# Performance work log

Measured on AMD Instinct MI355X. Metric: run time of the kernel, lower is better.

## Reference

```python
import itertools
import jax, jax.numpy as jnp
import numpy as np

B, S, D = 512, 49, 448
H, KD, RATIO, RES = 8, 32, 4, 7
EKD = KD * RATIO              # expanded key dim = 128
QKV_OUT = H * (2 * KD + EKD)  # 1536
MLP_HID = D * 4               # 1792
EPS = 1e-5
LS_INIT = 1e-5


def _build_bias_idxs():
    points = list(itertools.product(range(RES), range(RES)))
    offsets = {}
    idxs = []
    for p1 in points:
        for p2 in points:
            off = (abs(p1[0] - p2[0]), abs(p1[1] - p2[1]))
            if off not in offsets:
                offsets[off] = len(offsets)
            idxs.append(offsets[off])
    return np.asarray(idxs, dtype=np.int32).reshape(len(points), len(points)), len(offsets)


def setup_inputs() -> dict:
    key = jax.random.key(0)
    ks = jax.random.split(key, 10)
    idxs_np, n_off = _build_bias_idxs()  # (49,49), 49 unique offsets
    std = 0.02
    return {
        "hidden_states": jax.random.normal(ks[0], (B, S, D), jnp.float32),
        "ln1_g": jnp.ones((D,), jnp.float32),
        "ln1_b": jnp.zeros((D,), jnp.float32),
        "qkv_w": jax.random.normal(ks[1], (D, QKV_OUT), jnp.float32) * std,
        "qkv_b": jnp.zeros((QKV_OUT,), jnp.float32),
        "attention_biases": jax.random.normal(ks[2], (H, n_off), jnp.float32) * std,
        "proj_w": jax.random.normal(ks[3], (H * EKD, D), jnp.float32) * std,
        "proj_b": jnp.zeros((D,), jnp.float32),
        "ln2_g": jnp.ones((D,), jnp.float32),
        "ln2_b": jnp.zeros((D,), jnp.float32),
        "mlp_w1": jax.random.normal(ks[4], (D, MLP_HID), jnp.float32) * std,
        "mlp_b1": jnp.zeros((MLP_HID,), jnp.float32),
        "mlp_w2": jax.random.normal(ks[5], (MLP_HID, D), jnp.float32) * std,
        "mlp_b2": jnp.zeros((D,), jnp.float32),
        "ls1": jnp.full((D,), LS_INIT, jnp.float32),
        "ls2": jnp.full((D,), LS_INIT, jnp.float32),
        "attention_bias_idxs": jnp.asarray(idxs_np),
    }


def _layernorm(x, g, b):
    mu = jnp.mean(x, axis=-1, keepdims=True)
    var = jnp.mean(jnp.square(x - mu), axis=-1, keepdims=True)
    return (x - mu) * jax.lax.rsqrt(var + EPS) * g + b


def reference(hidden_states, ln1_g, ln1_b, qkv_w, qkv_b, attention_biases,
              proj_w, proj_b, ln2_g, ln2_b, mlp_w1, mlp_b1, mlp_w2, mlp_b2,
              ls1, ls2, attention_bias_idxs):
    x = hidden_states
    # --- token mixer (self-attention with relative-position bias) ---
    h = _layernorm(x, ln1_g, ln1_b)
    qkv = h @ qkv_w + qkv_b                           # [B,S,1536]
    qkv = qkv.reshape(B, S, H, 2 * KD + EKD)
    q, k, v = jnp.split(qkv, [KD, 2 * KD], axis=3)    # [B,S,H,32/32/128]
    scale = KD ** (-0.5)
    scores = jnp.einsum("bqhd,bkhd->bhqk", q, k) * scale
    bias = attention_biases[:, attention_bias_idxs]   # [H,S,S]
    probs = jax.nn.softmax(scores + bias[None], axis=-1)
    ctx = jnp.einsum("bhqk,bkhd->bqhd", probs, v).reshape(B, S, H * EKD)
    attn_out = ctx @ proj_w + proj_b                  # [B,S,D]
    # --- residual with layerscale (drop_path = identity in eval) ---
    x = x + ls1 * attn_out
    # --- MLP branch ---
    h2 = _layernorm(x, ln2_g, ln2_b)
    m = jax.nn.gelu(h2 @ mlp_w1 + mlp_b1, approximate=False)
    m = m @ mlp_w2 + mlp_b2
    x = x + ls2 * m
    return x
```

## Files before the change

kernel.cpp:

```cpp
#include <hip/hip_runtime.h>
#include <hip/hip_bf16.h>

#define BB 512
#define SS 49
#define DD 448
#define HH 8
#define QKVO 1536
#define MLPH 1792
#define MM (BB*SS)

using bf16_t = __hip_bfloat16;
typedef __attribute__((ext_vector_type(8))) short short8;
typedef __attribute__((ext_vector_type(4))) float f32x4;

__device__ __forceinline__ void gload_lds16(const void* g, void* l) {
  __builtin_amdgcn_global_load_lds(
      (const __attribute__((address_space(1))) void*)g,
      (__attribute__((address_space(3))) void*)l,
      16, 0, 0);
}

__global__ void prep_kernel(const float* __restrict__ qkv_w, const float* __restrict__ proj_w,
                            const float* __restrict__ w1, const float* __restrict__ w2,
                            const float* __restrict__ ab, const int* __restrict__ idxs,
                            bf16_t* __restrict__ qkv_wT, bf16_t* __restrict__ proj_wT,
                            bf16_t* __restrict__ w1T, bf16_t* __restrict__ w2T,
                            bf16_t* __restrict__ bias_pad)
{
  int idx = blockIdx.x * 256 + threadIdx.x;
  if (idx < 688128) {
    int n = idx / 448, k = idx % 448;
    qkv_wT[idx] = __float2bfloat16(qkv_w[k*1536 + n]);
  } else if ((idx -= 688128) < 458752) {
    int n = idx / 1024, k = idx % 1024;
    proj_wT[idx] = __float2bfloat16(proj_w[k*448 + n]);
  } else if ((idx -= 458752) < 802816) {
    int n = idx / 448, k = idx % 448;
    w1T[idx] = __float2bfloat16(w1[k*1792 + n]);
  } else if ((idx -= 802816) < 802816) {
    int n = idx / 1792, k = idx % 1792;
    w2T[idx] = __float2bfloat16(w2[k*448 + n]);
  } else if ((idx -= 802816) < 32768) {
    int h = idx >> 12, r = (idx >> 6) & 63, c = idx & 63;
    float v = (r < SS && c < SS) ? ab[h*49 + idxs[r*49 + c]] : -1e30f;
    bias_pad[idx] = __float2bfloat16(v);
  }
}

__global__ __launch_bounds__(256) void ln_kernel(const float* __restrict__ x,
                                                 const float* __restrict__ g,
                                                 const float* __restrict__ b,
                                                 bf16_t* __restrict__ out)
{
  const int w = threadIdx.x >> 6, lane = threadIdx.x & 63;
  const int row = blockIdx.x * 4 + w;
  const float* xr = x + (size_t)row * DD;
  float v[7];
  float s = 0.f;
#pragma unroll
  for (int j = 0; j < 7; ++j) { v[j] = xr[lane + 64*j]; s += v[j]; }
#pragma unroll
  for (int off = 32; off; off >>= 1) s += __shfl_xor(s, off, 64);
  const float mu = s * (1.0f/448.0f);
  float q = 0.f;
#pragma unroll
  for (int j = 0; j < 7; ++j) { float d = v[j] - mu; q += d*d; }
#pragma unroll
  for (int off = 32; off; off >>= 1) q += __shfl_xor(q, off, 64);
  const float rstd = rsqrtf(q * (1.0f/448.0f) + 1e-5f);
  bf16_t* orow = out + (size_t)row * DD;
#pragma unroll
  for (int j = 0; j < 7; ++j) {
    int c = lane + 64*j;
    orow[c] = __float2bfloat16((v[j] - mu) * rstd * g[c] + b[c]);
  }
}

enum { EP_BF16 = 0, EP_RES1 = 1, EP_GELU = 2, EP_RES2 = 3 };

template<int EPI>
__global__ __launch_bounds__(256, 2) void gemm_bf16(
    const bf16_t* __restrict__ A, const bf16_t* __restrict__ Bt,
    const float* __restrict__ bias, const float* __restrict__ resid,
    const float* __restrict__ ls, bf16_t* __restrict__ Obf,
    float* __restrict__ Of, int N, int K)
{
  __shared__ __align__(16) char lds[32768];
  const int t = threadIdx.x;
  const int lane = t & 63;
  const int w = t >> 6;
  const int m0 = blockIdx.x * 128;
  const int n0 = blockIdx.y * 128;
  const int fr = lane & 15;
  const int fq = lane >> 4;
  const int wm = (w >> 1) * 64;
  const int wn = (w & 1) * 64;

  f32x4 acc[4][4];
#pragma unroll
  for (int i = 0; i < 4; ++i)
#pragma unroll
    for (int j = 0; j < 4; ++j)
      acc[i][j] = f32x4{0.f, 0.f, 0.f, 0.f};

  const int rsub = t >> 3;
  const int g8 = (t & 7) ^ (rsub & 7);
  const int wbase = (t & 192) * 16;
  const int nkt = K >> 6;

  for (int kt = 0; kt < nkt; ++kt) {
    const int k0 = kt << 6;
#pragma unroll
    for (int i = 0; i < 4; ++i) {
      const int ra = i*32 + rsub;
      gload_lds16(A + (size_t)(m0 + ra) * K + (k0 + g8*8), lds + i*4096 + wbase);
      int rb = n0 + i*32 + rsub;
      if (rb >= N) rb = N - 1;
      gload_lds16(Bt + (size_t)rb * K + (k0 + g8*8), lds + 16384 + i*4096 + wbase);
    }
    __syncthreads();
#pragma unroll
    for (int kk = 0; kk < 2; ++kk) {
      short8 af[4], bfr[4];
#pragma unroll
      for (int i = 0; i < 4; ++i) {
        const int ra = wm + i*16 + fr;
        const int ca = (fq + kk*4) ^ (ra & 7);
        af[i] = *(const short8*)(lds + ra*128 + ca*16);
        const int rb2 = wn + i*16 + fr;
        const int cb = (fq + kk*4) ^ (rb2 & 7);
        bfr[i] = *(const short8*)(lds + 16384 + rb2*128 + cb*16);
      }
#pragma unroll
      for (int mi = 0; mi < 4; ++mi)
#pragma unroll
        for (int ni = 0; ni < 4; ++ni)
          acc[mi][ni] = __builtin_amdgcn_mfma_f32_16x16x32_bf16(af[mi], bfr[ni], acc[mi][ni], 0, 0, 0);
    }
    __syncthreads();
  }

#pragma unroll
  for (int mi = 0; mi < 4; ++mi) {
#pragma unroll
    for (int ni = 0; ni < 4; ++ni) {
      const int col = n0 + wn + ni*16 + fr;
      if (col < N) {
        const float bc = bias[col];
        const int row0 = m0 + wm + mi*16 + fq*4;
#pragma unroll
        for (int ri = 0; ri < 4; ++ri) {
          const size_t o = (size_t)(row0 + ri) * N + col;
          const float v = acc[mi][ni][ri] + bc;
          if constexpr (EPI == EP_BF16) {
            Obf[o] = __float2bfloat16(v);
          } else if constexpr (EPI == EP_GELU) {
            Obf[o] = __float2bfloat16(0.5f * v * (1.0f + erff(v * 0.7071067811865475f)));
          } else if constexpr (EPI == EP_RES1) {
            Of[o] = resid[o] + ls[col] * v;
          } else {
            Of[o] = Of[o] + ls[col] * v;
          }
        }
      }
    }
  }
}

__global__ __launch_bounds__(64) void attn_mfma_kernel(const bf16_t* __restrict__ qkv,
                                                       const bf16_t* __restrict__ bias_pad,
                                                       bf16_t* __restrict__ ctx)
{
  __shared__ __align__(16) bf16_t VsF[64*128];
  __shared__ __align__(16) bf16_t PsF[64*72];
  const int b = blockIdx.x >> 3, h = blockIdx.x & 7;
  const int l = threadIdx.x;
  const int fr = l & 15, g = l >> 4;
  const size_t base = ((size_t)b * SS) * QKVO + (size_t)h * 192;

  for (int c = l; c < 1024; c += 64) {
    const int j = c >> 4, ch = c & 15;
    const int jc = j < SS ? j : SS - 1;
    short8 v = *(const short8*)(qkv + base + (size_t)jc * QKVO + 64 + ch*8);
    *(short8*)(&VsF[j*128 + ((ch ^ (j >> 3)) & 15)*8]) = v;
  }

  short8 qf[4], kf[4];
#pragma unroll
  for (int mi = 0; mi < 4; ++mi) {
    int qr = mi*16 + fr; if (qr > SS-1) qr = SS-1;
    qf[mi] = *(const short8*)(qkv + base + (size_t)qr * QKVO + g*8);
    int kr = mi*16 + fr; if (kr > SS-1) kr = SS-1;
    kf[mi] = *(const short8*)(qkv + base + (size_t)kr * QKVO + 32 + g*8);
  }
  f32x4 sc[4][4];
#pragma unroll
  for (int mi = 0; mi < 4; ++mi)
#pragma unroll
    for (int ni = 0; ni < 4; ++ni)
      sc[mi][ni] = f32x4{0.f,0.f,0.f,0.f};
#pragma unroll
  for (int mi = 0; mi < 4; ++mi)
#pragma unroll
    for (int ni = 0; ni < 4; ++ni)
      sc[mi][ni] = __builtin_amdgcn_mfma_f32_16x16x32_bf16(qf[mi], kf[ni], sc[mi][ni], 0, 0, 0);

  const float scale = 0.17677669529663687f;
  const bf16_t* bp = bias_pad + (size_t)h * 4096;
#pragma unroll
  for (int mi = 0; mi < 4; ++mi) {
#pragma unroll
    for (int ri = 0; ri < 4; ++ri) {
      const int r = mi*16 + g*4 + ri;
      float v0 = sc[mi][0][ri]*scale + __bfloat162float(bp[r*64 +      fr]);
      float v1 = sc[mi][1][ri]*scale + __bfloat162float(bp[r*64 + 16 + fr]);
      float v2 = sc[mi][2][ri]*scale + __bfloat162float(bp[r*64 + 32 + fr]);
      float v3 = sc[mi][3][ri]*scale + __bfloat162float(bp[r*64 + 48 + fr]);
      float m = fmaxf(fmaxf(v0, v1), fmaxf(v2, v3));
#pragma unroll
      for (int off = 8; off; off >>= 1) m = fmaxf(m, __shfl_xor(m, off, 64));
      v0 = __expf(v0 - m); v1 = __expf(v1 - m);
      v2 = __expf(v2 - m); v3 = __expf(v3 - m);
      float s = v0 + v1 + v2 + v3;
#pragma unroll
      for (int off = 8; off; off >>= 1) s += __shfl_xor(s, off, 64);
      const float inv = 1.0f / s;
      PsF[r*72 +      fr] = __float2bfloat16(v0 * inv);
      PsF[r*72 + 16 + fr] = __float2bfloat16(v1 * inv);
      PsF[r*72 + 32 + fr] = __float2bfloat16(v2 * inv);
      PsF[r*72 + 48 + fr] = __float2bfloat16(v3 * inv);
    }
  }
  __syncthreads();

  short8 pf[4][2];
#pragma unroll
  for (int mi = 0; mi < 4; ++mi)
#pragma unroll
    for (int ks = 0; ks < 2; ++ks)
      pf[mi][ks] = *(const short8*)(&PsF[(mi*16 + fr)*72 + ks*32 + g*8]);

#pragma unroll
  for (int ni = 0; ni < 8; ++ni) {
    const int e = ni*16 + fr;
    short8 vf[2];
#pragma unroll
    for (int ks = 0; ks < 2; ++ks) {
      const int jb = ks*32 + g*8;
#pragma unroll
      for (int jj = 0; jj < 8; ++jj) {
        const int j = jb + jj;
        const int ch = ((e >> 3) ^ (j >> 3)) & 15;
        vf[ks][jj] = *(const short*)(&VsF[j*128 + ch*8 + (e & 7)]);
      }
    }
    f32x4 acc2[4];
#pragma unroll
    for (int mi = 0; mi < 4; ++mi) acc2[mi] = f32x4{0.f,0.f,0.f,0.f};
#pragma unroll
    for (int ks = 0; ks < 2; ++ks)
#pragma unroll
      for (int mi = 0; mi < 4; ++mi)
        acc2[mi] = __builtin_amdgcn_mfma_f32_16x16x32_bf16(pf[mi][ks], vf[ks], acc2[mi], 0, 0, 0);
#pragma unroll
    for (int mi = 0; mi < 4; ++mi) {
#pragma unroll
      for (int ri = 0; ri < 4; ++ri) {
        const int q = mi*16 + g*4 + ri;
        if (q < SS)
          ctx[((size_t)b * SS + q) * 1024 + h*128 + e] = __float2bfloat16(acc2[mi][ri]);
      }
    }
  }
}

extern "C" void kernel_launch(void* const* d_in, const int* in_sizes, int n_in,
                              void* d_out, int out_size, void* d_ws, size_t ws_size,
                              hipStream_t stream) {
  const float* x      = (const float*)d_in[0];
  const float* ln1_g  = (const float*)d_in[1];
  const float* ln1_b  = (const float*)d_in[2];
  const float* qkv_w  = (const float*)d_in[3];
  const float* qkv_b  = (const float*)d_in[4];
  const float* ab     = (const float*)d_in[5];
  const float* proj_w = (const float*)d_in[6];
  const float* proj_b = (const float*)d_in[7];
  const float* ln2_g  = (const float*)d_in[8];
  const float* ln2_b  = (const float*)d_in[9];
  const float* w1     = (const float*)d_in[10];
  const float* b1     = (const float*)d_in[11];
  const float* w2     = (const float*)d_in[12];
  const float* b2     = (const float*)d_in[13];
  const float* ls1    = (const float*)d_in[14];
  const float* ls2    = (const float*)d_in[15];
  const int*   idxs   = (const int*)d_in[16];
  float* out = (float*)d_out;
  char* ws = (char*)d_ws;

  bf16_t* h_buf    = (bf16_t*)(ws);
  bf16_t* qkv_buf  = (bf16_t*)(ws + 22478848);
  bf16_t* ctx_buf  = (bf16_t*)(ws + 99549184);
  bf16_t* m_buf    = (bf16_t*)(ws + 22478848);
  bf16_t* qkv_wT   = (bf16_t*)(ws + 150929408);
  bf16_t* proj_wT  = (bf16_t*)(ws + 152305664);
  bf16_t* w1T      = (bf16_t*)(ws + 153223168);
  bf16_t* w2T      = (bf16_t*)(ws + 154828800);
  bf16_t* bias_pad = (bf16_t*)(ws + 156434432);

  const int prep_total = 688128 + 458752 + 802816 + 802816 + 32768;
  prep_kernel<<<(prep_total + 255)/256, 256, 0, stream>>>(
      qkv_w, proj_w, w1, w2, ab, idxs, qkv_wT, proj_wT, w1T, w2T, bias_pad);

  ln_kernel<<<MM/4, 256, 0, stream>>>(x, ln1_g, ln1_b, h_buf);

  gemm_bf16<EP_BF16><<<dim3(MM/128, 12), 256, 0, stream>>>(
      h_buf, qkv_wT, qkv_b, nullptr, nullptr, qkv_buf, nullptr, QKVO, DD);

  attn_mfma_kernel<<<BB*HH, 64, 0, stream>>>(qkv_buf, bias_pad, ctx_buf);

  gemm_bf16<EP_RES1><<<dim3(MM/128, 4), 256, 0, stream>>>(
      ctx_buf, proj_wT, proj_b, x, ls1, nullptr, out, DD, 1024);

  ln_kernel<<<MM/4, 256, 0, stream>>>(out, ln2_g, ln2_b, h_buf);

  gemm_bf16<EP_GELU><<<dim3(MM/128, 14), 256, 0, stream>>>(
      h_buf, w1T, b1, nullptr, nullptr, m_buf, nullptr, MLPH, DD);

  gemm_bf16<EP_RES2><<<dim3(MM/128, 4), 256, 0, stream>>>(
      m_buf, w2T, b2, nullptr, ls2, nullptr, out, DD, MLPH);
}
```

Measured before the change: 342.9 us.

## Use 256x256 pipelined 8-wave GEMM and tiled transpose for weight prep

Replaces the 128x128 4-wave GEMM with a 256x256 tile, 512-thread kernel. It uses a 4-stage LDS ring buffer (128KB of dynamic shared memory), prefetches two K-steps ahead with direct global-to-LDS loads, and interleaves the half-tile loads with MFMA bursts under explicit barriers and priority hints. Weight transposes move from an uncoalesced gather kernel to an LDS-tiled transpose-cast. The larger tiles leave fewer blocks and waste columns on N=448 (the 2x256 grid pads to 512), and the 128KB of LDS may restrict occupancy to one block per CU.

Result: slower. 407.8 us (+19.0%).

```diff
diff --git a/kernel.cpp b/kernel.cpp
--- a/kernel.cpp
+++ b/kernel.cpp
@@ -20,31 +20,30 @@
       16, 0, 0);
 }
 
-__global__ void prep_kernel(const float* __restrict__ qkv_w, const float* __restrict__ proj_w,
-                            const float* __restrict__ w1, const float* __restrict__ w2,
-                            const float* __restrict__ ab, const int* __restrict__ idxs,
-                            bf16_t* __restrict__ qkv_wT, bf16_t* __restrict__ proj_wT,
-                            bf16_t* __restrict__ w1T, bf16_t* __restrict__ w2T,
-                            bf16_t* __restrict__ bias_pad)
+__global__ __launch_bounds__(256) void transpose_cast(const float* __restrict__ src,
+                                                      bf16_t* __restrict__ dst,
+                                                      int R, int C)
+{
+  __shared__ float tile[32][33];
+  const int tx = threadIdx.x & 31, ty = threadIdx.x >> 5;
+  const int c0 = blockIdx.x * 32, r0 = blockIdx.y * 32;
+#pragma unroll
+  for (int i = 0; i < 4; ++i)
+    tile[ty + i*8][tx] = src[(size_t)(r0 + ty + i*8) * C + c0 + tx];
+  __syncthreads();
+#pragma unroll
+  for (int i = 0; i < 4; ++i)
+    dst[(size_t)(c0 + ty + i*8) * R + r0 + tx] = __float2bfloat16(tile[tx][ty + i*8]);
+}
+
+__global__ __launch_bounds__(256) void biasprep_kernel(const float* __restrict__ ab,
+                                                       const int* __restrict__ idxs,
+                                                       bf16_t* __restrict__ bias_pad)
 {
   int idx = blockIdx.x * 256 + threadIdx.x;
-  if (idx < 688128) {
-    int n = idx / 448, k = idx % 448;
-    qkv_wT[idx] = __float2bfloat16(qkv_w[k*1536 + n]);
-  } else if ((idx -= 688128) < 458752) {
-    int n = idx / 1024, k = idx % 1024;
-    proj_wT[idx] = __float2bfloat16(proj_w[k*448 + n]);
-  } else if ((idx -= 458752) < 802816) {
-    int n = idx / 448, k = idx % 448;
-    w1T[idx] = __float2bfloat16(w1[k*1792 + n]);
-  } else if ((idx -= 802816) < 802816) {
-    int n = idx / 1792, k = idx % 1792;
-    w2T[idx] = __float2bfloat16(w2[k*448 + n]);
-  } else if ((idx -= 802816) < 32768) {
-    int h = idx >> 12, r = (idx >> 6) & 63, c = idx & 63;
-    float v = (r < SS && c < SS) ? ab[h*49 + idxs[r*49 + c]] : -1e30f;
-    bias_pad[idx] = __float2bfloat16(v);
-  }
+  int h = idx >> 12, r = (idx >> 6) & 63, c = idx & 63;
+  float v = (r < SS && c < SS) ? ab[h*49 + idxs[r*49 + c]] : -1e30f;
+  bias_pad[idx] = __float2bfloat16(v);
 }
 
 __global__ __launch_bounds__(256) void ln_kernel(const float* __restrict__ x,
@@ -78,76 +77,130 @@
 
 enum { EP_BF16 = 0, EP_RES1 = 1, EP_GELU = 2, EP_RES2 = 3 };
 
+#define MFMA_ROW(mi, areg) \
+  acc[mi][0] = __builtin_amdgcn_mfma_f32_16x16x32_bf16(areg, b0, acc[mi][0], 0, 0, 0); \
+  acc[mi][1] = __builtin_amdgcn_mfma_f32_16x16x32_bf16(areg, b1, acc[mi][1], 0, 0, 0); \
+  acc[mi][2] = __builtin_amdgcn_mfma_f32_16x16x32_bf16(areg, b2, acc[mi][2], 0, 0, 0); \
+  acc[mi][3] = __builtin_amdgcn_mfma_f32_16x16x32_bf16(areg, b3, acc[mi][3], 0, 0, 0);
+
 template<int EPI>
-__global__ __launch_bounds__(256, 2) void gemm_bf16(
+__global__ __launch_bounds__(512, 2) void gemm8_bf16(
     const bf16_t* __restrict__ A, const bf16_t* __restrict__ Bt,
     const float* __restrict__ bias, const float* __restrict__ resid,
     const float* __restrict__ ls, bf16_t* __restrict__ Obf,
     float* __restrict__ Of, int N, int K)
 {
-  __shared__ __align__(16) char lds[32768];
+  extern __shared__ char lds[];
   const int t = threadIdx.x;
   const int lane = t & 63;
   const int w = t >> 6;
-  const int m0 = blockIdx.x * 128;
-  const int n0 = blockIdx.y * 128;
-  const int fr = lane & 15;
-  const int fq = lane >> 4;
-  const int wm = (w >> 1) * 64;
-  const int wn = (w & 1) * 64;
-
-  f32x4 acc[4][4];
-#pragma unroll
-  for (int i = 0; i < 4; ++i)
+  const int wm = w >> 2, wn = w & 3;
+  const int m0 = blockIdx.x * 256;
+  const int n0 = blockIdx.y * 256;
+  const int NT = K >> 5;
+
+  const int fr = lane & 15, g = lane >> 4;
+  const int xs = (g ^ (fr & 3) ^ ((fr >> 2) & 1)) << 4;
+  const int fro = fr * 64 + xs;
+
+  const int r0s = w * 16 + (lane >> 2);
+  const int cc = lane & 3;
+  const int fq = cc ^ ((r0s & 3) ^ ((r0s >> 2) & 1));
+  const size_t gA0 = (size_t)(m0 + r0s) * K + fq * 8;
+  const size_t gA1 = gA0 + (size_t)128 * K;
+  int nb0 = n0 + r0s;       if (nb0 > N - 1) nb0 = N - 1;
+  int nb1 = n0 + 128 + r0s; if (nb1 > N - 1) nb1 = N - 1;
+  const size_t gB0 = (size_t)nb0 * K + fq * 8;
+  const size_t gB1 = (size_t)nb1 * K + fq * 8;
+  const int ldsw = w * 1024;
+
+  f32x4 acc[8][4];
+#pragma unroll
+  for (int i = 0; i < 8; ++i)
 #pragma unroll
     for (int j = 0; j < 4; ++j)
       acc[i][j] = f32x4{0.f, 0.f, 0.f, 0.f};
 
-  const int rsub = t >> 3;
-  const int g8 = (t & 7) ^ (rsub & 7);
-  const int wbase = (t & 192) * 16;
-  const int nkt = K >> 6;
-
-  for (int kt = 0; kt < nkt; ++kt) {
-    const int k0 = kt << 6;
-#pragma unroll
-    for (int i = 0; i < 4; ++i) {
-      const int ra = i*32 + rsub;
-      gload_lds16(A + (size_t)(m0 + ra) * K + (k0 + g8*8), lds + i*4096 + wbase);
-      int rb = n0 + i*32 + rsub;
-      if (rb >= N) rb = N - 1;
-      gload_lds16(Bt + (size_t)rb * K + (k0 + g8*8), lds + 16384 + i*4096 + wbase);
-    }
-    __syncthreads();
-#pragma unroll
-    for (int kk = 0; kk < 2; ++kk) {
-      short8 af[4], bfr[4];
-#pragma unroll
-      for (int i = 0; i < 4; ++i) {
-        const int ra = wm + i*16 + fr;
-        const int ca = (fq + kk*4) ^ (ra & 7);
-        af[i] = *(const short8*)(lds + ra*128 + ca*16);
-        const int rb2 = wn + i*16 + fr;
-        const int cb = (fq + kk*4) ^ (rb2 & 7);
-        bfr[i] = *(const short8*)(lds + 16384 + rb2*128 + cb*16);
-      }
-#pragma unroll
-      for (int mi = 0; mi < 4; ++mi)
-#pragma unroll
-        for (int ni = 0; ni < 4; ++ni)
-          acc[mi][ni] = __builtin_amdgcn_mfma_f32_16x16x32_bf16(af[mi], bfr[ni], acc[mi][ni], 0, 0, 0);
-    }
-    __syncthreads();
-  }
-
-#pragma unroll
-  for (int mi = 0; mi < 4; ++mi) {
+#pragma unroll
+  for (int T = 0; T < 2; ++T) {
+    char* sb = lds + T * 32768;
+    gload_lds16(A  + gA0 + T*32, sb + ldsw);
+    gload_lds16(Bt + gB0 + T*32, sb + 16384 + ldsw);
+    gload_lds16(A  + gA1 + T*32, sb + 8192 + ldsw);
+    gload_lds16(Bt + gB1 + T*32, sb + 16384 + 8192 + ldsw);
+  }
+  asm volatile("s_waitcnt vmcnt(4)" ::: "memory");
+  __builtin_amdgcn_sched_barrier(0);
+  __builtin_amdgcn_s_barrier();
+  __builtin_amdgcn_sched_barrier(0);
+
+  for (int T = 0; T < NT; ++T) {
+    const char* sb = lds + (T & 3) * 32768;
+    const char* sA = sb + wm * 8192 + fro;
+    const char* sB = sb + 16384 + wn * 4096 + fro;
+    const bool st = (T + 2 < NT);
+    const size_t ko = (size_t)(T + 2) * 32;
+    char* db = lds + ((T + 2) & 3) * 32768;
+
+    short8 a0 = *(const short8*)(sA);
+    short8 a1 = *(const short8*)(sA + 1024);
+    short8 a2 = *(const short8*)(sA + 2048);
+    short8 a3 = *(const short8*)(sA + 3072);
+    short8 b0 = *(const short8*)(sB);
+    short8 b1 = *(const short8*)(sB + 1024);
+    short8 b2 = *(const short8*)(sB + 2048);
+    short8 b3 = *(const short8*)(sB + 3072);
+    if (st) {
+      gload_lds16(A  + gA0 + ko, db + ldsw);
+      gload_lds16(Bt + gB0 + ko, db + 16384 + ldsw);
+    }
+    __builtin_amdgcn_sched_barrier(0);
+    __builtin_amdgcn_s_barrier();
+    asm volatile("s_waitcnt lgkmcnt(0)" ::: "memory");
+    __builtin_amdgcn_sched_barrier(0);
+    __builtin_amdgcn_s_setprio(1);
+    MFMA_ROW(0, a0)
+    MFMA_ROW(1, a1)
+    MFMA_ROW(2, a2)
+    MFMA_ROW(3, a3)
+    __builtin_amdgcn_s_setprio(0);
+    __builtin_amdgcn_sched_barrier(0);
+    __builtin_amdgcn_s_barrier();
+    __builtin_amdgcn_sched_barrier(0);
+
+    a0 = *(const short8*)(sA + 4096);
+    a1 = *(const short8*)(sA + 5120);
+    a2 = *(const short8*)(sA + 6144);
+    a3 = *(const short8*)(sA + 7168);
+    if (st) {
+      gload_lds16(A  + gA1 + ko, db + 8192 + ldsw);
+      gload_lds16(Bt + gB1 + ko, db + 16384 + 8192 + ldsw);
+    }
+    __builtin_amdgcn_sched_barrier(0);
+    __builtin_amdgcn_s_barrier();
+    asm volatile("s_waitcnt lgkmcnt(0)" ::: "memory");
+    __builtin_amdgcn_sched_barrier(0);
+    __builtin_amdgcn_s_setprio(1);
+    MFMA_ROW(4, a0)
+    MFMA_ROW(5, a1)
+    MFMA_ROW(6, a2)
+    MFMA_ROW(7, a3)
+    __builtin_amdgcn_s_setprio(0);
+    __builtin_amdgcn_sched_barrier(0);
+    if (st) { asm volatile("s_waitcnt vmcnt(4)" ::: "memory"); }
+    else    { asm volatile("s_waitcnt vmcnt(0)" ::: "memory"); }
+    __builtin_amdgcn_s_barrier();
+    __builtin_amdgcn_sched_barrier(0);
+  }
+
+#pragma unroll
+  for (int mi = 0; mi < 8; ++mi) {
 #pragma unroll
     for (int ni = 0; ni < 4; ++ni) {
-      const int col = n0 + wn + ni*16 + fr;
+      const int col = n0 + wn*64 + ni*16 + fr;
       if (col < N) {
         const float bc = bias[col];
-        const int row0 = m0 + wm + mi*16 + fq*4;
+        const int row0 = m0 + wm*128 + mi*16 + g*4;
 #pragma unroll
         for (int ri = 0; ri < 4; ++ri) {
           const size_t o = (size_t)(row0 + ri) * N + col;
@@ -307,25 +360,32 @@
   bf16_t* w2T      = (bf16_t*)(ws + 154828800);
   bf16_t* bias_pad = (bf16_t*)(ws + 156434432);
 
-  const int prep_total = 688128 + 458752 + 802816 + 802816 + 32768;
-  prep_kernel<<<(prep_total + 255)/256, 256, 0, stream>>>(
-      qkv_w, proj_w, w1, w2, ab, idxs, qkv_wT, proj_wT, w1T, w2T, bias_pad);
+  hipFuncSetAttribute((const void*)&gemm8_bf16<EP_BF16>, hipFuncAttributeMaxDynamicSharedMemorySize, 131072);
+  hipFuncSetAttribute((const void*)&gemm8_bf16<EP_RES1>, hipFuncAttributeMaxDynamicSharedMemorySize, 131072);
+  hipFuncSetAttribute((const void*)&gemm8_bf16<EP_GELU>, hipFuncAttributeMaxDynamicSharedMemorySize, 131072);
+  hipFuncSetAttribute((const void*)&gemm8_bf16<EP_RES2>, hipFuncAttributeMaxDynamicSharedMemorySize, 131072);
+
+  transpose_cast<<<dim3(QKVO/32, DD/32),  256, 0, stream>>>(qkv_w,  qkv_wT,  DD,   QKVO);
+  transpose_cast<<<dim3(DD/32, 1024/32),  256, 0, stream>>>(proj_w, proj_wT, 1024, DD);
+  transpose_cast<<<dim3(MLPH/32, DD/32),  256, 0, stream>>>(w1,     w1T,     DD,   MLPH);
+  transpose_cast<<<dim3(DD/32, MLPH/32),  256, 0, stream>>>(w2,     w2T,     MLPH, DD);
+  biasprep_kernel<<<128, 256, 0, stream>>>(ab, idxs, bias_pad);
 
   ln_kernel<<<MM/4, 256, 0, stream>>>(x, ln1_g, ln1_b, h_buf);
 
-  gemm_bf16<EP_BF16><<<dim3(MM/128, 12), 256, 0, stream>>>(
+  gemm8_bf16<EP_BF16><<<dim3(MM/256, QKVO/256), 512, 131072, stream>>>(
       h_buf, qkv_wT, qkv_b, nullptr, nullptr, qkv_buf, nullptr, QKVO, DD);
 
   attn_mfma_kernel<<<BB*HH, 64, 0, stream>>>(qkv_buf, bias_pad, ctx_buf);
 
-  gemm_bf16<EP_RES1><<<dim3(MM/128, 4), 256, 0, stream>>>(
+  gemm8_bf16<EP_RES1><<<dim3(MM/256, 2), 512, 131072, stream>>>(
       ctx_buf, proj_wT, proj_b, x, ls1, nullptr, out, DD, 1024);
 
   ln_kernel<<<MM/4, 256, 0, stream>>>(out, ln2_g, ln2_b, h_buf);
 
-  gemm_bf16<EP_GELU><<<dim3(MM/128, 14), 256, 0, stream>>>(
+  gemm8_bf16<EP_GELU><<<dim3(MM/256, MLPH/256), 512, 131072, stream>>>(
       h_buf, w1T, b1, nullptr, nullptr, m_buf, nullptr, MLPH, DD);
 
-  gemm_bf16<EP_RES2><<<dim3(MM/128, 4), 256, 0, stream>>>(
+  gemm8_bf16<EP_RES2><<<dim3(MM/256, 2), 512, 131072, stream>>>(
       m_buf, w2T, b2, nullptr, ls2, nullptr, out, DD, MLPH);
 }
```

## Triple-buffer GEMM LDS loads with async prefetch and tile weight transposes

Applied to the files above, without the earlier changes.

The GEMM kernel now uses a three-stage LDS ring with K-step 32. Loads are issued two tiles ahead through global_load_lds and gated by partial vmcnt waits, with a single barrier per iteration and raised MFMA priority. This is meant to hide global-load latency that the old load/sync/compute/sync loop exposed. Separately, the monolithic weight prep kernel is split into shared-memory tiled transpose-cast kernels so that reads are coalesced. The trade-off is 48KB of LDS per block, which may limit occupancy, along with a new swizzle scheme and more hand-written waitcnt logic to keep correct.

New measurement: 400.2 us. +16.7%, slower.

```diff
diff --git a/kernel.cpp b/kernel.cpp
--- a/kernel.cpp
+++ b/kernel.cpp
@@ -20,31 +20,30 @@
       16, 0, 0);
 }
 
-__global__ void prep_kernel(const float* __restrict__ qkv_w, const float* __restrict__ proj_w,
-                            const float* __restrict__ w1, const float* __restrict__ w2,
-                            const float* __restrict__ ab, const int* __restrict__ idxs,
-                            bf16_t* __restrict__ qkv_wT, bf16_t* __restrict__ proj_wT,
-                            bf16_t* __restrict__ w1T, bf16_t* __restrict__ w2T,
-                            bf16_t* __restrict__ bias_pad)
+__global__ __launch_bounds__(256) void transpose_cast(const float* __restrict__ src,
+                                                      bf16_t* __restrict__ dst,
+                                                      int R, int C)
+{
+  __shared__ float tile[32][33];
+  const int tx = threadIdx.x & 31, ty = threadIdx.x >> 5;
+  const int c0 = blockIdx.x * 32, r0 = blockIdx.y * 32;
+#pragma unroll
+  for (int i = 0; i < 4; ++i)
+    tile[ty + i*8][tx] = src[(size_t)(r0 + ty + i*8) * C + c0 + tx];
+  __syncthreads();
+#pragma unroll
+  for (int i = 0; i < 4; ++i)
+    dst[(size_t)(c0 + ty + i*8) * R + r0 + tx] = __float2bfloat16(tile[tx][ty + i*8]);
+}
+
+__global__ __launch_bounds__(256) void biasprep_kernel(const float* __restrict__ ab,
+                                                       const int* __restrict__ idxs,
+                                                       bf16_t* __restrict__ bias_pad)
 {
   int idx = blockIdx.x * 256 + threadIdx.x;
-  if (idx < 688128) {
-    int n = idx / 448, k = idx % 448;
-    qkv_wT[idx] = __float2bfloat16(qkv_w[k*1536 + n]);
-  } else if ((idx -= 688128) < 458752) {
-    int n = idx / 1024, k = idx % 1024;
-    proj_wT[idx] = __float2bfloat16(proj_w[k*448 + n]);
-  } else if ((idx -= 458752) < 802816) {
-    int n = idx / 448, k = idx % 448;
-    w1T[idx] = __float2bfloat16(w1[k*1792 + n]);
-  } else if ((idx -= 802816) < 802816) {
-    int n = idx / 1792, k = idx % 1792;
-    w2T[idx] = __float2bfloat16(w2[k*448 + n]);
-  } else if ((idx -= 802816) < 32768) {
-    int h = idx >> 12, r = (idx >> 6) & 63, c = idx & 63;
-    float v = (r < SS && c < SS) ? ab[h*49 + idxs[r*49 + c]] : -1e30f;
-    bias_pad[idx] = __float2bfloat16(v);
-  }
+  int h = idx >> 12, r = (idx >> 6) & 63, c = idx & 63;
+  float v = (r < SS && c < SS) ? ab[h*49 + idxs[r*49 + c]] : -1e30f;
+  bias_pad[idx] = __float2bfloat16(v);
 }
 
 __global__ __launch_bounds__(256) void ln_kernel(const float* __restrict__ x,
@@ -79,22 +78,42 @@
 enum { EP_BF16 = 0, EP_RES1 = 1, EP_GELU = 2, EP_RES2 = 3 };
 
 template<int EPI>
-__global__ __launch_bounds__(256, 2) void gemm_bf16(
+__global__ __launch_bounds__(256, 3) void gemmp_bf16(
     const bf16_t* __restrict__ A, const bf16_t* __restrict__ Bt,
     const float* __restrict__ bias, const float* __restrict__ resid,
     const float* __restrict__ ls, bf16_t* __restrict__ Obf,
     float* __restrict__ Of, int N, int K)
 {
-  __shared__ __align__(16) char lds[32768];
+  __shared__ __align__(16) char lds[49152];
   const int t = threadIdx.x;
   const int lane = t & 63;
   const int w = t >> 6;
   const int m0 = blockIdx.x * 128;
   const int n0 = blockIdx.y * 128;
-  const int fr = lane & 15;
-  const int fq = lane >> 4;
-  const int wm = (w >> 1) * 64;
-  const int wn = (w & 1) * 64;
+  const int NT = K >> 5;
+  const int fr = lane & 15, g = lane >> 4;
+  const int wm = (w >> 1) * 64, wn = (w & 1) * 64;
+  const int xs = (g ^ (fr & 3) ^ ((fr >> 2) & 1)) << 4;
+
+  int aoff[4], boff[4];
+#pragma unroll
+  for (int i = 0; i < 4; ++i) {
+    aoff[i] = (wm + i*16 + fr) * 64 + xs;
+    boff[i] = 8192 + (wn + i*16 + fr) * 64 + xs;
+  }
+
+  const int p = t & 3;
+  const bf16_t* srcA[2];
+  const bf16_t* srcB[2];
+#pragma unroll
+  for (int i = 0; i < 2; ++i) {
+    const int r = i*64 + (t >> 2);
+    const int l = p ^ (r & 3) ^ ((r >> 2) & 1);
+    srcA[i] = A + (size_t)(m0 + r) * K + l*8;
+    int rb = n0 + r; if (rb > N - 1) rb = N - 1;
+    srcB[i] = Bt + (size_t)rb * K + l*8;
+  }
+  const int wb = w * 1024;
 
   f32x4 acc[4][4];
 #pragma unroll
@@ -103,41 +122,51 @@
     for (int j = 0; j < 4; ++j)
       acc[i][j] = f32x4{0.f, 0.f, 0.f, 0.f};
 
-  const int rsub = t >> 3;
-  const int g8 = (t & 7) ^ (rsub & 7);
-  const int wbase = (t & 192) * 16;
-  const int nkt = K >> 6;
-
-  for (int kt = 0; kt < nkt; ++kt) {
-    const int k0 = kt << 6;
+#pragma unroll
+  for (int T = 0; T < 2; ++T) {
+    char* sb = lds + T * 16384;
+    gload_lds16(srcA[0] + T*32, sb + wb);
+    gload_lds16(srcA[1] + T*32, sb + 4096 + wb);
+    gload_lds16(srcB[0] + T*32, sb + 8192 + wb);
+    gload_lds16(srcB[1] + T*32, sb + 12288 + wb);
+  }
+  asm volatile("s_waitcnt vmcnt(4)" ::: "memory");
+  __builtin_amdgcn_sched_barrier(0);
+  asm volatile("s_barrier" ::: "memory");
+  __builtin_amdgcn_sched_barrier(0);
+
+  int sl = 0;
+  for (int T = 0; T < NT; ++T) {
+    const char* sb = lds + sl * 16384;
+    const bool st = (T + 2 < NT);
+    if (st) {
+      int sl2 = sl + 2; if (sl2 >= 3) sl2 -= 3;
+      char* db = lds + sl2 * 16384;
+      const int ko = (T + 2) * 32;
+      gload_lds16(srcA[0] + ko, db + wb);
+      gload_lds16(srcA[1] + ko, db + 4096 + wb);
+      gload_lds16(srcB[0] + ko, db + 8192 + wb);
+      gload_lds16(srcB[1] + ko, db + 12288 + wb);
+    }
+    short8 af[4], bf_[4];
 #pragma unroll
     for (int i = 0; i < 4; ++i) {
-      const int ra = i*32 + rsub;
-      gload_lds16(A + (size_t)(m0 + ra) * K + (k0 + g8*8), lds + i*4096 + wbase);
-      int rb = n0 + i*32 + rsub;
-      if (rb >= N) rb = N - 1;
-      gload_lds16(Bt + (size_t)rb * K + (k0 + g8*8), lds + 16384 + i*4096 + wbase);
-    }
-    __syncthreads();
-#pragma unroll
-    for (int kk = 0; kk < 2; ++kk) {
-      short8 af[4], bfr[4];
-#pragma unroll
-      for (int i = 0; i < 4; ++i) {
-        const int ra = wm + i*16 + fr;
-        const int ca = (fq + kk*4) ^ (ra & 7);
-        af[i] = *(const short8*)(lds + ra*128 + ca*16);
-        const int rb2 = wn + i*16 + fr;
-        const int cb = (fq + kk*4) ^ (rb2 & 7);
-        bfr[i] = *(const short8*)(lds + 16384 + rb2*128 + cb*16);
-      }
-#pragma unroll
-      for (int mi = 0; mi < 4; ++mi)
-#pragma unroll
-        for (int ni = 0; ni < 4; ++ni)
-          acc[mi][ni] = __builtin_amdgcn_mfma_f32_16x16x32_bf16(af[mi], bfr[ni], acc[mi][ni], 0, 0, 0);
-    }
-    __syncthreads();
+      af[i]  = *(const short8*)(sb + aoff[i]);
+      bf_[i] = *(const short8*)(sb + boff[i]);
+    }
+    __builtin_amdgcn_s_setprio(1);
+#pragma unroll
+    for (int mi = 0; mi < 4; ++mi)
+#pragma unroll
+      for (int ni = 0; ni < 4; ++ni)
+        acc[mi][ni] = __builtin_amdgcn_mfma_f32_16x16x32_bf16(af[mi], bf_[ni], acc[mi][ni], 0, 0, 0);
+    __builtin_amdgcn_s_setprio(0);
+    __builtin_amdgcn_sched_barrier(0);
+    if (st) { asm volatile("s_waitcnt vmcnt(4)" ::: "memory"); }
+    else    { asm volatile("s_waitcnt vmcnt(0)" ::: "memory"); }
+    asm volatile("s_barrier" ::: "memory");
+    __builtin_amdgcn_sched_barrier(0);
+    sl = (sl + 1 == 3) ? 0 : sl + 1;
   }
 
 #pragma unroll
@@ -147,7 +176,7 @@
       const int col = n0 + wn + ni*16 + fr;
       if (col < N) {
         const float bc = bias[col];
-        const int row0 = m0 + wm + mi*16 + fq*4;
+        const int row0 = m0 + wm + mi*16 + g*4;
 #pragma unroll
         for (int ri = 0; ri < 4; ++ri) {
           const size_t o = (size_t)(row0 + ri) * N + col;
@@ -307,25 +336,27 @@
   bf16_t* w2T      = (bf16_t*)(ws + 154828800);
   bf16_t* bias_pad = (bf16_t*)(ws + 156434432);
 
-  const int prep_total = 688128 + 458752 + 802816 + 802816 + 32768;
-  prep_kernel<<<(prep_total + 255)/256, 256, 0, stream>>>(
-      qkv_w, proj_w, w1, w2, ab, idxs, qkv_wT, proj_wT, w1T, w2T, bias_pad);
+  transpose_cast<<<dim3(QKVO/32, DD/32),  256, 0, stream>>>(qkv_w,  qkv_wT,  DD,   QKVO);
+  transpose_cast<<<dim3(DD/32, 1024/32),  256, 0, stream>>>(proj_w, proj_wT, 1024, DD);
+  transpose_cast<<<dim3(MLPH/32, DD/32),  256, 0, stream>>>(w1,     w1T,     DD,   MLPH);
+  transpose_cast<<<dim3(DD/32, MLPH/32),  256, 0, stream>>>(w2,     w2T,     MLPH, DD);
+  biasprep_kernel<<<128, 256, 0, stream>>>(ab, idxs, bias_pad);
 
   ln_kernel<<<MM/4, 256, 0, stream>>>(x, ln1_g, ln1_b, h_buf);
 
-  gemm_bf16<EP_BF16><<<dim3(MM/128, 12), 256, 0, stream>>>(
+  gemmp_bf16<EP_BF16><<<dim3(MM/128, QKVO/128), 256, 0, stream>>>(
       h_buf, qkv_wT, qkv_b, nullptr, nullptr, qkv_buf, nullptr, QKVO, DD);
 
   attn_mfma_kernel<<<BB*HH, 64, 0, stream>>>(qkv_buf, bias_pad, ctx_buf);
 
-  gemm_bf16<EP_RES1><<<dim3(MM/128, 4), 256, 0, stream>>>(
+  gemmp_bf16<EP_RES1><<<dim3(MM/128, 4), 256, 0, stream>>>(
       ctx_buf, proj_wT, proj_b, x, ls1, nullptr, out, DD, 1024);
 
   ln_kernel<<<MM/4, 256, 0, stream>>>(out, ln2_g, ln2_b, h_buf);
 
-  gemm_bf16<EP_GELU><<<dim3(MM/128, 14), 256, 0, stream>>>(
+  gemmp_bf16<EP_GELU><<<dim3(MM/128, MLPH/128), 256, 0, stream>>>(
       h_buf, w1T, b1, nullptr, nullptr, m_buf, nullptr, MLPH, DD);
 
-  gemm_bf16<EP_RES2><<<dim3(MM/128, 4), 256, 0, stream>>>(
+  gemmp_bf16<EP_RES2><<<dim3(MM/128, 4), 256, 0, stream>>>(
       m_buf, w2T, b2, nullptr, ls2, nullptr, out, DD, MLPH);
 }
```

## Tile weight transposes, swizzle GEMM block order, use 64-row tiles for narrow GEMMs

Applied to the files above, without the earlier changes.

Replaces the naive strided weight transpose-cast with an LDS-tiled transpose kernel per weight, and moves bias table prep into its own kernel. GEMMs now use a 1D grid with an XCD-aware block swizzle so neighbouring tiles share the same die's L2. The two N=448 GEMMs switch to 64-row M tiles, which doubles their block count for better CU occupancy. The cost is more launches, and the smaller tiles reuse each B load less.

Result: faster. 324.4 us (-5.4%).

```diff
diff --git a/kernel.cpp b/kernel.cpp
--- a/kernel.cpp
+++ b/kernel.cpp
@@ -20,31 +20,30 @@
       16, 0, 0);
 }
 
-__global__ void prep_kernel(const float* __restrict__ qkv_w, const float* __restrict__ proj_w,
-                            const float* __restrict__ w1, const float* __restrict__ w2,
-                            const float* __restrict__ ab, const int* __restrict__ idxs,
-                            bf16_t* __restrict__ qkv_wT, bf16_t* __restrict__ proj_wT,
-                            bf16_t* __restrict__ w1T, bf16_t* __restrict__ w2T,
-                            bf16_t* __restrict__ bias_pad)
+__global__ __launch_bounds__(256) void transpose_cast(const float* __restrict__ src,
+                                                      bf16_t* __restrict__ dst,
+                                                      int R, int C)
+{
+  __shared__ float tile[32][33];
+  const int tx = threadIdx.x & 31, ty = threadIdx.x >> 5;
+  const int c0 = blockIdx.x * 32, r0 = blockIdx.y * 32;
+#pragma unroll
+  for (int i = 0; i < 4; ++i)
+    tile[ty + i*8][tx] = src[(size_t)(r0 + ty + i*8) * C + c0 + tx];
+  __syncthreads();
+#pragma unroll
+  for (int i = 0; i < 4; ++i)
+    dst[(size_t)(c0 + ty + i*8) * R + r0 + tx] = __float2bfloat16(tile[tx][ty + i*8]);
+}
+
+__global__ __launch_bounds__(256) void biasprep_kernel(const float* __restrict__ ab,
+                                                       const int* __restrict__ idxs,
+                                                       bf16_t* __restrict__ bias_pad)
 {
   int idx = blockIdx.x * 256 + threadIdx.x;
-  if (idx < 688128) {
-    int n = idx / 448, k = idx % 448;
-    qkv_wT[idx] = __float2bfloat16(qkv_w[k*1536 + n]);
-  } else if ((idx -= 688128) < 458752) {
-    int n = idx / 1024, k = idx % 1024;
-    proj_wT[idx] = __float2bfloat16(proj_w[k*448 + n]);
-  } else if ((idx -= 458752) < 802816) {
-    int n = idx / 448, k = idx % 448;
-    w1T[idx] = __float2bfloat16(w1[k*1792 + n]);
-  } else if ((idx -= 802816) < 802816) {
-    int n = idx / 1792, k = idx % 1792;
-    w2T[idx] = __float2bfloat16(w2[k*448 + n]);
-  } else if ((idx -= 802816) < 32768) {
-    int h = idx >> 12, r = (idx >> 6) & 63, c = idx & 63;
-    float v = (r < SS && c < SS) ? ab[h*49 + idxs[r*49 + c]] : -1e30f;
-    bias_pad[idx] = __float2bfloat16(v);
-  }
+  int h = idx >> 12, r = (idx >> 6) & 63, c = idx & 63;
+  float v = (r < SS && c < SS) ? ab[h*49 + idxs[r*49 + c]] : -1e30f;
+  bias_pad[idx] = __float2bfloat16(v);
 }
 
 __global__ __launch_bounds__(256) void ln_kernel(const float* __restrict__ x,
@@ -78,61 +77,72 @@
 
 enum { EP_BF16 = 0, EP_RES1 = 1, EP_GELU = 2, EP_RES2 = 3 };
 
-template<int EPI>
-__global__ __launch_bounds__(256, 2) void gemm_bf16(
+template<int EPI, int BM>
+__global__ __launch_bounds__(256, 2) void gemmr_bf16(
     const bf16_t* __restrict__ A, const bf16_t* __restrict__ Bt,
     const float* __restrict__ bias, const float* __restrict__ resid,
     const float* __restrict__ ls, bf16_t* __restrict__ Obf,
-    float* __restrict__ Of, int N, int K)
-{
-  __shared__ __align__(16) char lds[32768];
+    float* __restrict__ Of, int N, int K, int gy)
+{
+  constexpr int MI = BM / 32;
+  constexpr int ABYTES = BM * 128;
+  __shared__ __align__(16) char lds[ABYTES + 16384];
   const int t = threadIdx.x;
   const int lane = t & 63;
   const int w = t >> 6;
-  const int m0 = blockIdx.x * 128;
-  const int n0 = blockIdx.y * 128;
+
+  const int chunk = gridDim.x >> 3;
+  const int lin = blockIdx.x;
+  const int swz = (lin & 7) * chunk + (lin >> 3);
+  const int m0 = (swz / gy) * BM;
+  const int n0 = (swz % gy) * 128;
+
   const int fr = lane & 15;
   const int fq = lane >> 4;
-  const int wm = (w >> 1) * 64;
+  const int wm = (w >> 1) * (BM / 2);
   const int wn = (w & 1) * 64;
 
-  f32x4 acc[4][4];
-#pragma unroll
-  for (int i = 0; i < 4; ++i)
+  f32x4 acc[MI][4];
+#pragma unroll
+  for (int i = 0; i < MI; ++i)
 #pragma unroll
     for (int j = 0; j < 4; ++j)
       acc[i][j] = f32x4{0.f, 0.f, 0.f, 0.f};
 
   const int rsub = t >> 3;
   const int g8 = (t & 7) ^ (rsub & 7);
-  const int wbase = (t & 192) * 16;
+  const int wbase = w * 1024;
   const int nkt = K >> 6;
 
   for (int kt = 0; kt < nkt; ++kt) {
     const int k0 = kt << 6;
 #pragma unroll
+    for (int i = 0; i < MI; ++i)
+      gload_lds16(A + (size_t)(m0 + i*32 + rsub) * K + (k0 + g8*8), lds + i*4096 + wbase);
+#pragma unroll
     for (int i = 0; i < 4; ++i) {
-      const int ra = i*32 + rsub;
-      gload_lds16(A + (size_t)(m0 + ra) * K + (k0 + g8*8), lds + i*4096 + wbase);
       int rb = n0 + i*32 + rsub;
       if (rb >= N) rb = N - 1;
-      gload_lds16(Bt + (size_t)rb * K + (k0 + g8*8), lds + 16384 + i*4096 + wbase);
+      gload_lds16(Bt + (size_t)rb * K + (k0 + g8*8), lds + ABYTES + i*4096 + wbase);
     }
     __syncthreads();
 #pragma unroll
     for (int kk = 0; kk < 2; ++kk) {
-      short8 af[4], bfr[4];
-#pragma unroll
-      for (int i = 0; i < 4; ++i) {
+      short8 af[MI], bfr[4];
+#pragma unroll
+      for (int i = 0; i < MI; ++i) {
         const int ra = wm + i*16 + fr;
         const int ca = (fq + kk*4) ^ (ra & 7);
         af[i] = *(const short8*)(lds + ra*128 + ca*16);
+      }
+#pragma unroll
+      for (int i = 0; i < 4; ++i) {
         const int rb2 = wn + i*16 + fr;
         const int cb = (fq + kk*4) ^ (rb2 & 7);
-        bfr[i] = *(const short8*)(lds + 16384 + rb2*128 + cb*16);
-      }
-#pragma unroll
-      for (int mi = 0; mi < 4; ++mi)
+        bfr[i] = *(const short8*)(lds + ABYTES + rb2*128 + cb*16);
+      }
+#pragma unroll
+      for (int mi = 0; mi < MI; ++mi)
 #pragma unroll
         for (int ni = 0; ni < 4; ++ni)
           acc[mi][ni] = __builtin_amdgcn_mfma_f32_16x16x32_bf16(af[mi], bfr[ni], acc[mi][ni], 0, 0, 0);
@@ -141,7 +151,7 @@
   }
 
 #pragma unroll
-  for (int mi = 0; mi < 4; ++mi) {
+  for (int mi = 0; mi < MI; ++mi) {
 #pragma unroll
     for (int ni = 0; ni < 4; ++ni) {
       const int col = n0 + wn + ni*16 + fr;
@@ -307,25 +317,27 @@
   bf16_t* w2T      = (bf16_t*)(ws + 154828800);
   bf16_t* bias_pad = (bf16_t*)(ws + 156434432);
 
-  const int prep_total = 688128 + 458752 + 802816 + 802816 + 32768;
-  prep_kernel<<<(prep_total + 255)/256, 256, 0, stream>>>(
-      qkv_w, proj_w, w1, w2, ab, idxs, qkv_wT, proj_wT, w1T, w2T, bias_pad);
+  transpose_cast<<<dim3(QKVO/32, DD/32),  256, 0, stream>>>(qkv_w,  qkv_wT,  DD,   QKVO);
+  transpose_cast<<<dim3(DD/32, 1024/32),  256, 0, stream>>>(proj_w, proj_wT, 1024, DD);
+  transpose_cast<<<dim3(MLPH/32, DD/32),  256, 0, stream>>>(w1,     w1T,     DD,   MLPH);
+  transpose_cast<<<dim3(DD/32, MLPH/32),  256, 0, stream>>>(w2,     w2T,     MLPH, DD);
+  biasprep_kernel<<<128, 256, 0, stream>>>(ab, idxs, bias_pad);
 
   ln_kernel<<<MM/4, 256, 0, stream>>>(x, ln1_g, ln1_b, h_buf);
 
-  gemm_bf16<EP_BF16><<<dim3(MM/128, 12), 256, 0, stream>>>(
-      h_buf, qkv_wT, qkv_b, nullptr, nullptr, qkv_buf, nullptr, QKVO, DD);
+  gemmr_bf16<EP_BF16, 128><<<196*12, 256, 0, stream>>>(
+      h_buf, qkv_wT, qkv_b, nullptr, nullptr, qkv_buf, nullptr, QKVO, DD, 12);
 
   attn_mfma_kernel<<<BB*HH, 64, 0, stream>>>(qkv_buf, bias_pad, ctx_buf);
 
-  gemm_bf16<EP_RES1><<<dim3(MM/128, 4), 256, 0, stream>>>(
-      ctx_buf, proj_wT, proj_b, x, ls1, nullptr, out, DD, 1024);
+  gemmr_bf16<EP_RES1, 64><<<392*4, 256, 0, stream>>>(
+      ctx_buf, proj_wT, proj_b, x, ls1, nullptr, out, DD, 1024, 4);
 
   ln_kernel<<<MM/4, 256, 0, stream>>>(out, ln2_g, ln2_b, h_buf);
 
-  gemm_bf16<EP_GELU><<<dim3(MM/128, 14), 256, 0, stream>>>(
-      h_buf, w1T, b1, nullptr, nullptr, m_buf, nullptr, MLPH, DD);
-
-  gemm_bf16<EP_RES2><<<dim3(MM/128, 4), 256, 0, stream>>>(
-      m_buf, w2T, b2, nullptr, ls2, nullptr, out, DD, MLPH);
-}
+  gemmr_bf16<EP_GELU, 128><<<196*14, 256, 0, stream>>>(
+      h_buf, w1T, b1, nullptr, nullptr, m_buf, nullptr, MLPH, DD, 14);
+
+  gemmr_bf16<EP_RES2, 64><<<392*4, 256, 0, stream>>>(
+      m_buf, w2T, b2, nullptr, ls2, nullptr, out, DD, MLPH, 4);
+}
```
